# Performance work log

Hardware: AMD Instinct MI355X
Metric: run time of the kernel (lower is better)

The kernel has to match this reference:

```python
import jax, jax.numpy as jnp
import numpy as np

B, C, T, F_, H, HID = 4, 128, 400, 64, 4, 32
CV = C // H  # per-head value channels
EPS = 1e-5


def _head_conv_act_norm(x, W, b, p, g, z):
    # x: [N, C, 2, F]; W: [H, O, C]; b: [H, O]; p: [H] (PReLU); g,z: [H, O, F]
    y = jnp.einsum('hoc,nctf->hnotf', W, x) + b[:, None, :, None, None]
    y = jnp.where(y >= 0, y, p[:, None, None, None, None] * y)  # PReLU (single param per module)
    # LayerNormalization4D over (channel, freq) per (n, t), affine [O, F]
    mu = y.mean(axis=(2, 4), keepdims=True)
    var = y.var(axis=(2, 4), keepdims=True)
    y = (y - mu) / jnp.sqrt(var + EPS)
    return y * g[:, None, :, None, :] + z[:, None, :, None, :]  # [H, N, O, 2, F]


def _conv_act_norm(x, W, b, p, g, z):
    # x: [N, C, 2, F]; W: [O, C]; p: scalar; g,z: [O, F]
    y = jnp.einsum('oc,nctf->notf', W, x) + b[None, :, None, None]
    y = jnp.where(y >= 0, y, p * y)
    mu = y.mean(axis=(1, 3), keepdims=True)
    var = y.var(axis=(1, 3), keepdims=True)
    y = (y - mu) / jnp.sqrt(var + EPS)
    return y * g[None, :, None, :] + z[None, :, None, :]


def setup_inputs() -> dict:
    key = jax.random.key(0)
    ks = jax.random.split(key, 10)
    s = 0.02
    inp = {
        'x1': jax.random.normal(ks[0], (B, C, T, F_), jnp.float32),
        'x2': jax.random.normal(ks[1], (B, C, T, F_), jnp.float32),
        # Query branches (per head)
        'Wq': jax.random.normal(ks[2], (H, HID, C), jnp.float32) * s,
        'bq': jnp.zeros((H, HID), jnp.float32),
        'pq': jnp.full((H,), 0.25, jnp.float32),
        'gq': jnp.ones((H, HID, F_), jnp.float32),
        'zq': jnp.zeros((H, HID, F_), jnp.float32),
        # Key branches
        'Wk': jax.random.normal(ks[3], (H, HID, C), jnp.float32) * s,
        'bk': jnp.zeros((H, HID), jnp.float32),
        'pk': jnp.full((H,), 0.25, jnp.float32),
        'gk': jnp.ones((H, HID, F_), jnp.float32),
        'zk': jnp.zeros((H, HID, F_), jnp.float32),
        # Value branches
        'Wv': jax.random.normal(ks[4], (H, CV, C), jnp.float32) * s,
        'bv': jnp.zeros((H, CV), jnp.float32),
        'pv': jnp.full((H,), 0.25, jnp.float32),
        'gv': jnp.ones((H, CV, F_), jnp.float32),
        'zv': jnp.zeros((H, CV, F_), jnp.float32),
        # Output concat projection
        'Wo': jax.random.normal(ks[5], (C, C), jnp.float32) * s,
        'bo': jnp.zeros((C,), jnp.float32),
        'po': jnp.asarray(0.25, jnp.float32),
        'go': jnp.ones((C, F_), jnp.float32),
        'zo': jnp.zeros((C, F_), jnp.float32),
    }
    return inp


def reference(x1, x2, Wq, bq, pq, gq, zq, Wk, bk, pk, gk, zk, Wv, bv, pv, gv, zv, Wo, bo, po, go, zo):
    N = B * T
    # [B,C,T,F] -> [B*T, C, F]; stack the two streams along a tiny seq axis of 2
    a = x1.transpose(0, 2, 1, 3).reshape(N, C, F_)
    b = x2.transpose(0, 2, 1, 3).reshape(N, C, F_)
    x = jnp.stack([a, b], axis=2)  # [N, C, 2, F]

    Q = _head_conv_act_norm(x, Wq, bq, pq, gq, zq)  # [H, N, HID, 2, F]
    K = _head_conv_act_norm(x, Wk, bk, pk, gk, zk)
    V = _head_conv_act_norm(x, Wv, bv, pv, gv, zv)  # [H, N, CV, 2, F]

    d = HID * F_
    q = Q.transpose(0, 1, 3, 2, 4).reshape(H, N, 2, d)
    k = K.transpose(0, 1, 3, 2, 4).reshape(H, N, 2, d)
    v = V.transpose(0, 1, 3, 2, 4).reshape(H, N, 2, CV * F_)

    attn = jax.nn.softmax(jnp.einsum('hnsd,hntd->hnst', q, k) / (d ** 0.5), axis=-1)  # [H,N,2,2]
    o = jnp.einsum('hnst,hntd->hnsd', attn, v)  # [H, N, 2, CV*F]
    # [H,N,2,CV,F] -> [N, H*CV, 2, F]
    o = o.reshape(H, N, 2, CV, F_).transpose(1, 0, 3, 2, 4).reshape(N, C, 2, F_)

    out = _conv_act_norm(o, Wo, bo, po, go, zo)  # [N, C, 2, F]

    y1 = out[:, :, 0, :].reshape(B, T, C, F_).transpose(0, 2, 1, 3) + x1
    y2 = out[:, :, 1, :].reshape(B, T, C, F_).transpose(0, 2, 1, 3) + x2
    return (y1, y2)
```

## Files before the change

### kernel.cpp

```cpp
#include <hip/hip_runtime.h>


typedef short s8v __attribute__((ext_vector_type(8)));
typedef float f4v __attribute__((ext_vector_type(4)));

__device__ __forceinline__ unsigned short f2bf(float x){
  unsigned u = __float_as_uint(x);
  return (unsigned short)((u + 0x7FFFu + ((u >> 16) & 1u)) >> 16);
}
__device__ __forceinline__ float b2f(unsigned short b){
  return __uint_as_float(((unsigned)b) << 16);
}
__device__ __forceinline__ float wred(float v){
  #pragma unroll
  for (int off = 32; off; off >>= 1) v += __shfl_xor(v, off, 64);
  return v;
}

__global__ __launch_bounds__(256)
void prep_k(const float* __restrict__ Wq, const float* __restrict__ Wk,
            const float* __restrict__ Wv, const float* __restrict__ Wo,
            const float* __restrict__ gq, const float* __restrict__ zq,
            const float* __restrict__ gk, const float* __restrict__ zk,
            const float* __restrict__ gv, const float* __restrict__ zv,
            const float* __restrict__ go, const float* __restrict__ zo,
            unsigned short* __restrict__ Wb, unsigned* __restrict__ GZ)
{
  int t = blockIdx.x * 256 + threadIdx.x;
  if (t < 65536) {
    int sel = t >> 14, i = t & 16383;
    const float* s = sel == 0 ? Wq : sel == 1 ? Wk : sel == 2 ? Wv : Wo;
    Wb[t] = f2bf(s[i]);
  } else {
    int u = t - 65536;
    int sel = u >> 13, i = u & 8191;
    const float* g = sel == 0 ? gq : sel == 1 ? gk : sel == 2 ? gv : go;
    const float* z = sel == 0 ? zq : sel == 1 ? zk : sel == 2 ? zv : zo;
    GZ[u] = (unsigned)f2bf(g[i]) | ((unsigned)f2bf(z[i]) << 16);
  }
}

__device__ __forceinline__ void gemm_tile(const unsigned short* __restrict__ A,
                                          const unsigned short* __restrict__ Bl,
                                          int m0, int n0, int row16, int q4,
                                          f4v acc[2][4])
{
  #pragma unroll
  for (int mi = 0; mi < 2; ++mi)
    #pragma unroll
    for (int ni = 0; ni < 4; ++ni)
      acc[mi][ni] = (f4v){0.f, 0.f, 0.f, 0.f};

  #pragma unroll
  for (int kk = 0; kk < 4; ++kk) {
    s8v a[2];
    #pragma unroll
    for (int mi = 0; mi < 2; ++mi)
      a[mi] = *(const s8v*)(A + (m0 + mi*16 + row16)*128 + kk*32 + q4*8);
    #pragma unroll
    for (int ni = 0; ni < 4; ++ni) {
      int rw = n0 + ni*16 + row16;
      const s8v b = *(const s8v*)(Bl + rw*128 + ((kk*32 + q4*8) ^ ((rw & 7) << 3)));
      #pragma unroll
      for (int mi = 0; mi < 2; ++mi)
        acc[mi][ni] = __builtin_amdgcn_mfma_f32_16x16x32_bf16(a[mi], b, acc[mi][ni], 0, 0, 0);
    }
  }
}

__device__ __forceinline__ void qkv_epi(f4v acc[2][4],
                                        const float* __restrict__ bias,
                                        float p,
                                        const unsigned* __restrict__ GZb,
                                        unsigned short* __restrict__ Lout, bool keep,
                                        int m0, int n0, int row16, int q4)
{
  float sum = 0.f, sq = 0.f;
  #pragma unroll
  for (int mi = 0; mi < 2; ++mi) {
    #pragma unroll
    for (int j = 0; j < 4; ++j) {
      float bb = bias[m0 + mi*16 + q4*4 + j];
      #pragma unroll
      for (int ni = 0; ni < 4; ++ni) {
        float v = acc[mi][ni][j] + bb;
        v = v >= 0.f ? v : p * v;
        acc[mi][ni][j] = v;
        sum += v; sq += v*v;
      }
    }
  }
  sum = wred(sum); sq = wred(sq);
  float mu = sum * (1.f/2048.f);
  float rs = rsqrtf(sq * (1.f/2048.f) - mu*mu + 1e-5f);
  #pragma unroll
  for (int mi = 0; mi < 2; ++mi) {
    #pragma unroll
    for (int ni = 0; ni < 4; ++ni) {
      int f   = ni*16 + row16;
      int col = n0 + f;
      int sw  = (col & 7) << 3;
      #pragma unroll
      for (int j = 0; j < 4; ++j) {
        int r = m0 + mi*16 + q4*4 + j;
        unsigned gz = GZb[r*64 + f];
        float g = b2f((unsigned short)(gz & 0xffffu));
        float z = b2f((unsigned short)(gz >> 16));
        float vn = (acc[mi][ni][j] - mu) * rs * g + z;
        if (keep) acc[mi][ni][j] = vn;
        else      Lout[col*128 + (r ^ sw)] = f2bf(vn);
      }
    }
  }
}

__global__ __launch_bounds__(512, 4)
void fused_k(const float* __restrict__ x1, const float* __restrict__ x2,
             const unsigned short* __restrict__ Wb, const unsigned* __restrict__ GZ,
             const float* __restrict__ bq, const float* __restrict__ bk,
             const float* __restrict__ bv, const float* __restrict__ bo,
             const float* __restrict__ pq, const float* __restrict__ pk,
             const float* __restrict__ pv, const float* __restrict__ po,
             float* __restrict__ out)
{
  __shared__ unsigned short Xl[16384];
  __shared__ unsigned short Kl[16384];
  __shared__ float sc[16];
  __shared__ float lnb[16];

  const int n   = blockIdx.x;
  const int bI  = n / 400, tI = n % 400;
  const int tid = threadIdx.x;
  const int lane = tid & 63, wave = tid >> 6;
  const int wm = wave >> 1, wn = wave & 1;
  const int m0 = wm * 32, n0 = wn * 64;
  const int row16 = lane & 15, q4 = lane >> 4;

  {
    int c = tid & 127, s = (tid >> 7) & 1, half = tid >> 8;
    const float* src = (s ? x2 : x1) + ((size_t)(bI*128 + c)*400 + tI)*64 + half*32;
    #pragma unroll
    for (int j = 0; j < 8; ++j) {
      float4 v = ((const float4*)src)[j];
      int f0 = half*32 + j*4;
      float vv[4] = {v.x, v.y, v.z, v.w};
      #pragma unroll
      for (int e = 0; e < 4; ++e) {
        int rw = s*64 + f0 + e;
        Xl[rw*128 + (c ^ ((rw & 7) << 3))] = f2bf(vv[e]);
      }
    }
  }
  __syncthreads();

  f4v acc[2][4];

  gemm_tile(Wb + 16384*1, Xl, m0, n0, row16, q4, acc);
  qkv_epi(acc, bk, pk[wm], GZ + 8192*1, Kl, false, m0, n0, row16, q4);
  __syncthreads();

  gemm_tile(Wb + 16384*0, Xl, m0, n0, row16, q4, acc);
  qkv_epi(acc, bq, pq[wm], GZ + 8192*0, Kl, true, m0, n0, row16, q4);
  {
    float p0 = 0.f, p1 = 0.f;
    #pragma unroll
    for (int mi = 0; mi < 2; ++mi) {
      #pragma unroll
      for (int ni = 0; ni < 4; ++ni) {
        int f  = ni*16 + row16;
        int sw = (f & 7) << 3;
        #pragma unroll
        for (int j = 0; j < 4; ++j) {
          int r = m0 + mi*16 + q4*4 + j;
          float qv = acc[mi][ni][j];
          float k0 = b2f(Kl[f*128      + (r ^ sw)]);
          float k1 = b2f(Kl[(64+f)*128 + (r ^ sw)]);
          p0 += qv * k0;
          p1 += qv * k1;
        }
      }
    }
    p0 = wred(p0); p1 = wred(p1);
    if (lane == 0) {
      sc[wm*4 + wn*2 + 0] = p0;
      sc[wm*4 + wn*2 + 1] = p1;
    }
  }
  __syncthreads();

  gemm_tile(Wb + 16384*2, Xl, m0, n0, row16, q4, acc);
  qkv_epi(acc, bv, pv[wm], GZ + 8192*2, Kl, false, m0, n0, row16, q4);
  __syncthreads();

  {
    const float is = 0.02209708691f;
    #pragma unroll
    for (int i = 0; i < 2; ++i) {
      int g  = tid + 512*i;
      int f  = g >> 4, cg = g & 15, c0 = cg*8, h = cg >> 2;
      float s00 = sc[h*4+0]*is, s01 = sc[h*4+1]*is;
      float s10 = sc[h*4+2]*is, s11 = sc[h*4+3]*is;
      float mA = fmaxf(s00, s01), e0 = __expf(s00-mA), e1 = __expf(s01-mA);
      float a00 = e0/(e0+e1), a01 = e1/(e0+e1);
      float mB = fmaxf(s10, s11), e2 = __expf(s10-mB), e3 = __expf(s11-mB);
      float a10 = e2/(e2+e3), a11 = e3/(e2+e3);
      int sw = (f & 7) << 3;
      int off0 = f*128      + (c0 ^ sw);
      int off1 = (64+f)*128 + (c0 ^ sw);
      s8v v0 = *(const s8v*)(Kl + off0);
      s8v v1 = *(const s8v*)(Kl + off1);
      s8v o0, o1;
      #pragma unroll
      for (int e = 0; e < 8; ++e) {
        float x0  = b2f((unsigned short)v0[e]);
        float x1v = b2f((unsigned short)v1[e]);
        o0[e] = (short)f2bf(a00*x0 + a01*x1v);
        o1[e] = (short)f2bf(a10*x0 + a11*x1v);
      }
      *(s8v*)(Kl + off0) = o0;
      *(s8v*)(Kl + off1) = o1;
    }
  }
  __syncthreads();

  gemm_tile(Wb + 16384*3, Kl, m0, n0, row16, q4, acc);
  {
    float pov = po[0];
    float sum = 0.f, sq = 0.f;
    #pragma unroll
    for (int mi = 0; mi < 2; ++mi) {
      #pragma unroll
      for (int j = 0; j < 4; ++j) {
        float bb = bo[m0 + mi*16 + q4*4 + j];
        #pragma unroll
        for (int ni = 0; ni < 4; ++ni) {
          float v = acc[mi][ni][j] + bb;
          v = v >= 0.f ? v : pov * v;
          acc[mi][ni][j] = v;
          sum += v; sq += v*v;
        }
      }
    }
    sum = wred(sum); sq = wred(sq);
    if (lane == 0) { lnb[wave] = sum; lnb[8 + wave] = sq; }
    __syncthreads();
    float tot  = lnb[wn]   + lnb[wn+2]   + lnb[wn+4]   + lnb[wn+6];
    float totq = lnb[8+wn] + lnb[8+wn+2] + lnb[8+wn+4] + lnb[8+wn+6];
    float mu = tot * (1.f/8192.f);
    float rs = rsqrtf(totq * (1.f/8192.f) - mu*mu + 1e-5f);
    const unsigned* GZo = GZ + 8192*3;
    float* outs = out + (size_t)wn * 13107200u;
    #pragma unroll
    for (int mi = 0; mi < 2; ++mi) {
      #pragma unroll
      for (int ni = 0; ni < 4; ++ni) {
        int f   = ni*16 + row16;
        int col = n0 + f;
        int sw  = (col & 7) << 3;
        #pragma unroll
        for (int j = 0; j < 4; ++j) {
          int r = m0 + mi*16 + q4*4 + j;
          unsigned gz = GZo[r*64 + f];
          float g = b2f((unsigned short)(gz & 0xffffu));
          float z = b2f((unsigned short)(gz >> 16));
          float y  = (acc[mi][ni][j] - mu) * rs * g + z;
          float xv = b2f(Xl[col*128 + (r ^ sw)]);
          outs[((size_t)(bI*128 + r)*400 + tI)*64 + f] = y + xv;
        }
      }
    }
  }
}

extern "C" void kernel_launch(void* const* d_in, const int* in_sizes, int n_in,
                              void* d_out, int out_size, void* d_ws, size_t ws_size,
                              hipStream_t stream)
{
  (void)in_sizes; (void)n_in; (void)out_size; (void)ws_size;
  const float* x1 = (const float*)d_in[0];
  const float* x2 = (const float*)d_in[1];
  const float* Wq = (const float*)d_in[2];
  const float* bq = (const float*)d_in[3];
  const float* pq = (const float*)d_in[4];
  const float* gq = (const float*)d_in[5];
  const float* zq = (const float*)d_in[6];
  const float* Wk = (const float*)d_in[7];
  const float* bk = (const float*)d_in[8];
  const float* pk = (const float*)d_in[9];
  const float* gk = (const float*)d_in[10];
  const float* zk = (const float*)d_in[11];
  const float* Wv = (const float*)d_in[12];
  const float* bv = (const float*)d_in[13];
  const float* pv = (const float*)d_in[14];
  const float* gv = (const float*)d_in[15];
  const float* zv = (const float*)d_in[16];
  const float* Wo = (const float*)d_in[17];
  const float* bo = (const float*)d_in[18];
  const float* po = (const float*)d_in[19];
  const float* go = (const float*)d_in[20];
  const float* zo = (const float*)d_in[21];

  unsigned short* Wb = (unsigned short*)d_ws;
  unsigned*       GZ = (unsigned*)((char*)d_ws + 131072);

  prep_k<<<384, 256, 0, stream>>>(Wq, Wk, Wv, Wo, gq, zq, gk, zk, gv, zv, go, zo, Wb, GZ);
  fused_k<<<1600, 512, 0, stream>>>(x1, x2, Wb, GZ, bq, bk, bv, bo, pq, pk, pv, po,
                                    (float*)d_out);
}
```

Baseline: 236.3 us.

## Split weights into bf16 hi/lo pairs, keep V in registers, stage output through LDS

Each weight is now stored as a bf16 high part plus a bf16 residual, and every GEMM issues two MFMAs per tile so the weight side is closer to fp32 accuracy. This doubles the MFMA work and the weight loads. The V attention mixing now happens in registers: one wave group hands its values over through fp32 LDS, so the bf16 round-trip through shared memory is gone. The final output is staged through LDS so each stream is written back with coalesced float4 stores instead of scattered scalar stores.

```diff
diff --git a/kernel.cpp b/kernel.cpp
--- a/kernel.cpp
+++ b/kernel.cpp
@@ -30,7 +30,10 @@
   if (t < 65536) {
     int sel = t >> 14, i = t & 16383;
     const float* s = sel == 0 ? Wq : sel == 1 ? Wk : sel == 2 ? Wv : Wo;
-    Wb[t] = f2bf(s[i]);
+    float w = s[i];
+    unsigned short hi = f2bf(w);
+    Wb[t]         = hi;
+    Wb[65536 + t] = f2bf(w - b2f(hi));
   } else {
     int u = t - 65536;
     int sel = u >> 13, i = u & 8191;
@@ -45,6 +48,7 @@
                                           int m0, int n0, int row16, int q4,
                                           f4v acc[2][4])
 {
+  const unsigned short* Al = A + 65536;
   #pragma unroll
   for (int mi = 0; mi < 2; ++mi)
     #pragma unroll
@@ -53,17 +57,22 @@
 
   #pragma unroll
   for (int kk = 0; kk < 4; ++kk) {
-    s8v a[2];
-    #pragma unroll
-    for (int mi = 0; mi < 2; ++mi)
-      a[mi] = *(const s8v*)(A + (m0 + mi*16 + row16)*128 + kk*32 + q4*8);
+    s8v ah[2], al[2];
+    #pragma unroll
+    for (int mi = 0; mi < 2; ++mi) {
+      int off = (m0 + mi*16 + row16)*128 + kk*32 + q4*8;
+      ah[mi] = *(const s8v*)(A  + off);
+      al[mi] = *(const s8v*)(Al + off);
+    }
     #pragma unroll
     for (int ni = 0; ni < 4; ++ni) {
       int rw = n0 + ni*16 + row16;
       const s8v b = *(const s8v*)(Bl + rw*128 + ((kk*32 + q4*8) ^ ((rw & 7) << 3)));
       #pragma unroll
-      for (int mi = 0; mi < 2; ++mi)
-        acc[mi][ni] = __builtin_amdgcn_mfma_f32_16x16x32_bf16(a[mi], b, acc[mi][ni], 0, 0, 0);
+      for (int mi = 0; mi < 2; ++mi) {
+        acc[mi][ni] = __builtin_amdgcn_mfma_f32_16x16x32_bf16(ah[mi], b, acc[mi][ni], 0, 0, 0);
+        acc[mi][ni] = __builtin_amdgcn_mfma_f32_16x16x32_bf16(al[mi], b, acc[mi][ni], 0, 0, 0);
+      }
     }
   }
 }
@@ -123,8 +132,8 @@
              const float* __restrict__ pv, const float* __restrict__ po,
              float* __restrict__ out)
 {
-  __shared__ unsigned short Xl[16384];
-  __shared__ unsigned short Kl[16384];
+  __shared__ __align__(16) unsigned short Xl[16384];
+  __shared__ __align__(16) unsigned short Kl[16384];
   __shared__ float sc[16];
   __shared__ float lnb[16];
 
@@ -189,39 +198,60 @@
   __syncthreads();
 
   gemm_tile(Wb + 16384*2, Xl, m0, n0, row16, q4, acc);
-  qkv_epi(acc, bv, pv[wm], GZ + 8192*2, Kl, false, m0, n0, row16, q4);
-  __syncthreads();
-
-  {
-    const float is = 0.02209708691f;
-    #pragma unroll
-    for (int i = 0; i < 2; ++i) {
-      int g  = tid + 512*i;
-      int f  = g >> 4, cg = g & 15, c0 = cg*8, h = cg >> 2;
-      float s00 = sc[h*4+0]*is, s01 = sc[h*4+1]*is;
-      float s10 = sc[h*4+2]*is, s11 = sc[h*4+3]*is;
+  qkv_epi(acc, bv, pv[wm], GZ + 8192*2, Kl, true, m0, n0, row16, q4);
+
+  {
+    float* KlF = (float*)Kl;
+    if (wn == 0) {
+      #pragma unroll
+      for (int mi = 0; mi < 2; ++mi)
+        #pragma unroll
+        for (int ni = 0; ni < 4; ++ni) {
+          int f = ni*16 + row16;
+          #pragma unroll
+          for (int j = 0; j < 4; ++j)
+            KlF[(m0 + mi*16 + q4*4 + j)*64 + f] = acc[mi][ni][j];
+        }
+    }
+    __syncthreads();
+    float v0r[2][4][4];
+    if (wn == 1) {
+      #pragma unroll
+      for (int mi = 0; mi < 2; ++mi)
+        #pragma unroll
+        for (int ni = 0; ni < 4; ++ni) {
+          int f = ni*16 + row16;
+          #pragma unroll
+          for (int j = 0; j < 4; ++j)
+            v0r[mi][ni][j] = KlF[(m0 + mi*16 + q4*4 + j)*64 + f];
+        }
+    }
+    __syncthreads();
+    if (wn == 1) {
+      const float is = 0.02209708691f;
+      float s00 = sc[wm*4+0]*is, s01 = sc[wm*4+1]*is;
+      float s10 = sc[wm*4+2]*is, s11 = sc[wm*4+3]*is;
       float mA = fmaxf(s00, s01), e0 = __expf(s00-mA), e1 = __expf(s01-mA);
       float a00 = e0/(e0+e1), a01 = e1/(e0+e1);
       float mB = fmaxf(s10, s11), e2 = __expf(s10-mB), e3 = __expf(s11-mB);
       float a10 = e2/(e2+e3), a11 = e3/(e2+e3);
-      int sw = (f & 7) << 3;
-      int off0 = f*128      + (c0 ^ sw);
-      int off1 = (64+f)*128 + (c0 ^ sw);
-      s8v v0 = *(const s8v*)(Kl + off0);
-      s8v v1 = *(const s8v*)(Kl + off1);
-      s8v o0, o1;
-      #pragma unroll
-      for (int e = 0; e < 8; ++e) {
-        float x0  = b2f((unsigned short)v0[e]);
-        float x1v = b2f((unsigned short)v1[e]);
-        o0[e] = (short)f2bf(a00*x0 + a01*x1v);
-        o1[e] = (short)f2bf(a10*x0 + a11*x1v);
-      }
-      *(s8v*)(Kl + off0) = o0;
-      *(s8v*)(Kl + off1) = o1;
-    }
-  }
-  __syncthreads();
+      #pragma unroll
+      for (int mi = 0; mi < 2; ++mi)
+        #pragma unroll
+        for (int ni = 0; ni < 4; ++ni) {
+          int f  = ni*16 + row16;
+          int sw = (f & 7) << 3;
+          #pragma unroll
+          for (int j = 0; j < 4; ++j) {
+            int c = m0 + mi*16 + q4*4 + j;
+            float v0 = v0r[mi][ni][j], v1 = acc[mi][ni][j];
+            Kl[f*128      + (c ^ sw)] = f2bf(a00*v0 + a01*v1);
+            Kl[(64+f)*128 + (c ^ sw)] = f2bf(a10*v0 + a11*v1);
+          }
+        }
+    }
+    __syncthreads();
+  }
 
   gemm_tile(Wb + 16384*3, Kl, m0, n0, row16, q4, acc);
   {
@@ -249,7 +279,6 @@
     float mu = tot * (1.f/8192.f);
     float rs = rsqrtf(totq * (1.f/8192.f) - mu*mu + 1e-5f);
     const unsigned* GZo = GZ + 8192*3;
-    float* outs = out + (size_t)wn * 13107200u;
     #pragma unroll
     for (int mi = 0; mi < 2; ++mi) {
       #pragma unroll
@@ -265,9 +294,40 @@
           float z = b2f((unsigned short)(gz >> 16));
           float y  = (acc[mi][ni][j] - mu) * rs * g + z;
           float xv = b2f(Xl[col*128 + (r ^ sw)]);
-          outs[((size_t)(bI*128 + r)*400 + tI)*64 + f] = y + xv;
-        }
-      }
+          acc[mi][ni][j] = y + xv;
+        }
+      }
+    }
+  }
+
+  {
+    float* KlF = (float*)Kl;
+    const size_t obase = ((size_t)bI * 128 * 400 + (size_t)tI) * 64;
+    #pragma unroll
+    for (int srnd = 0; srnd < 2; ++srnd) {
+      if (wn == srnd) {
+        #pragma unroll
+        for (int mi = 0; mi < 2; ++mi)
+          #pragma unroll
+          for (int ni = 0; ni < 4; ++ni) {
+            int f = ni*16 + row16;
+            #pragma unroll
+            for (int j = 0; j < 4; ++j) {
+              int r = m0 + mi*16 + q4*4 + j;
+              KlF[r*64 + f] = acc[mi][ni][j];
+            }
+          }
+      }
+      __syncthreads();
+      float* outs = out + (size_t)srnd * 13107200u + obase;
+      #pragma unroll
+      for (int k = 0; k < 4; ++k) {
+        int s = k*512 + tid;
+        int r = s >> 4, f4 = (s & 15) * 4;
+        float4 v = *(const float4*)(KlF + r*64 + f4);
+        *(float4*)(outs + (size_t)r * 25600 + f4) = v;
+      }
+      if (srnd == 0) __syncthreads();
     }
   }
 }
@@ -301,7 +361,7 @@
   const float* zo = (const float*)d_in[21];
 
   unsigned short* Wb = (unsigned short*)d_ws;
-  unsigned*       GZ = (unsigned*)((char*)d_ws + 131072);
+  unsigned*       GZ = (unsigned*)((char*)d_ws + 262144);
 
   prep_k<<<384, 256, 0, stream>>>(Wq, Wk, Wv, Wo, gq, zq, gk, zk, gv, zv, go, zo, Wb, GZ);
   fused_k<<<1600, 512, 0, stream>>>(x1, x2, Wb, GZ, bq, bk, bv, bo, pq, pk, pv, po,
```

Result: slower. 323.5 us (+36.9%).

## Split weights into hi/lo bf16 pairs, stage output through LDS for vector stores

Applied to the files above, without the earlier changes.

The weights are now stored as a high bf16 plus a low bf16 residual, and each GEMM issues two MFMAs per tile to recover near-fp32 weight precision. This doubles MFMA work and the A-operand loads. The final output is now written into LDS (reusing Kl as float) one wn-half at a time and then emitted as coalesced float4 nontemporal stores instead of scattered scalar stores. Input loads also switch to nontemporal float4 loads. The extra syncs and the doubled matrix math trade against the better output coalescing.

```diff
diff --git a/kernel.cpp b/kernel.cpp
--- a/kernel.cpp
+++ b/kernel.cpp
@@ -3,6 +3,7 @@
 
 typedef short s8v __attribute__((ext_vector_type(8)));
 typedef float f4v __attribute__((ext_vector_type(4)));
+typedef float fv4 __attribute__((ext_vector_type(4)));
 
 __device__ __forceinline__ unsigned short f2bf(float x){
   unsigned u = __float_as_uint(x);
@@ -30,7 +31,10 @@
   if (t < 65536) {
     int sel = t >> 14, i = t & 16383;
     const float* s = sel == 0 ? Wq : sel == 1 ? Wk : sel == 2 ? Wv : Wo;
-    Wb[t] = f2bf(s[i]);
+    float w = s[i];
+    unsigned short hi = f2bf(w);
+    Wb[t]         = hi;
+    Wb[65536 + t] = f2bf(w - b2f(hi));
   } else {
     int u = t - 65536;
     int sel = u >> 13, i = u & 8191;
@@ -45,6 +49,7 @@
                                           int m0, int n0, int row16, int q4,
                                           f4v acc[2][4])
 {
+  const unsigned short* Al = A + 65536;
   #pragma unroll
   for (int mi = 0; mi < 2; ++mi)
     #pragma unroll
@@ -53,17 +58,22 @@
 
   #pragma unroll
   for (int kk = 0; kk < 4; ++kk) {
-    s8v a[2];
-    #pragma unroll
-    for (int mi = 0; mi < 2; ++mi)
-      a[mi] = *(const s8v*)(A + (m0 + mi*16 + row16)*128 + kk*32 + q4*8);
+    s8v ah[2], al[2];
+    #pragma unroll
+    for (int mi = 0; mi < 2; ++mi) {
+      int off = (m0 + mi*16 + row16)*128 + kk*32 + q4*8;
+      ah[mi] = *(const s8v*)(A  + off);
+      al[mi] = *(const s8v*)(Al + off);
+    }
     #pragma unroll
     for (int ni = 0; ni < 4; ++ni) {
       int rw = n0 + ni*16 + row16;
       const s8v b = *(const s8v*)(Bl + rw*128 + ((kk*32 + q4*8) ^ ((rw & 7) << 3)));
       #pragma unroll
-      for (int mi = 0; mi < 2; ++mi)
-        acc[mi][ni] = __builtin_amdgcn_mfma_f32_16x16x32_bf16(a[mi], b, acc[mi][ni], 0, 0, 0);
+      for (int mi = 0; mi < 2; ++mi) {
+        acc[mi][ni] = __builtin_amdgcn_mfma_f32_16x16x32_bf16(ah[mi], b, acc[mi][ni], 0, 0, 0);
+        acc[mi][ni] = __builtin_amdgcn_mfma_f32_16x16x32_bf16(al[mi], b, acc[mi][ni], 0, 0, 0);
+      }
     }
   }
 }
@@ -123,8 +133,8 @@
              const float* __restrict__ pv, const float* __restrict__ po,
              float* __restrict__ out)
 {
-  __shared__ unsigned short Xl[16384];
-  __shared__ unsigned short Kl[16384];
+  __shared__ __align__(16) unsigned short Xl[16384];
+  __shared__ __align__(16) unsigned short Kl[16384];
   __shared__ float sc[16];
   __shared__ float lnb[16];
 
@@ -141,13 +151,12 @@
     const float* src = (s ? x2 : x1) + ((size_t)(bI*128 + c)*400 + tI)*64 + half*32;
     #pragma unroll
     for (int j = 0; j < 8; ++j) {
-      float4 v = ((const float4*)src)[j];
+      fv4 v = __builtin_nontemporal_load(((const fv4*)src) + j);
       int f0 = half*32 + j*4;
-      float vv[4] = {v.x, v.y, v.z, v.w};
       #pragma unroll
       for (int e = 0; e < 4; ++e) {
         int rw = s*64 + f0 + e;
-        Xl[rw*128 + (c ^ ((rw & 7) << 3))] = f2bf(vv[e]);
+        Xl[rw*128 + (c ^ ((rw & 7) << 3))] = f2bf(v[e]);
       }
     }
   }
@@ -249,7 +258,6 @@
     float mu = tot * (1.f/8192.f);
     float rs = rsqrtf(totq * (1.f/8192.f) - mu*mu + 1e-5f);
     const unsigned* GZo = GZ + 8192*3;
-    float* outs = out + (size_t)wn * 13107200u;
     #pragma unroll
     for (int mi = 0; mi < 2; ++mi) {
       #pragma unroll
@@ -265,9 +273,40 @@
           float z = b2f((unsigned short)(gz >> 16));
           float y  = (acc[mi][ni][j] - mu) * rs * g + z;
           float xv = b2f(Xl[col*128 + (r ^ sw)]);
-          outs[((size_t)(bI*128 + r)*400 + tI)*64 + f] = y + xv;
+          acc[mi][ni][j] = y + xv;
         }
       }
+    }
+  }
+
+  {
+    float* KlF = (float*)Kl;
+    const size_t obase = ((size_t)bI * 128 * 400 + (size_t)tI) * 64;
+    #pragma unroll
+    for (int srnd = 0; srnd < 2; ++srnd) {
+      if (wn == srnd) {
+        #pragma unroll
+        for (int mi = 0; mi < 2; ++mi)
+          #pragma unroll
+          for (int ni = 0; ni < 4; ++ni) {
+            int f = ni*16 + row16;
+            #pragma unroll
+            for (int j = 0; j < 4; ++j) {
+              int r = m0 + mi*16 + q4*4 + j;
+              KlF[r*64 + f] = acc[mi][ni][j];
+            }
+          }
+      }
+      __syncthreads();
+      float* outs = out + (size_t)srnd * 13107200u + obase;
+      #pragma unroll
+      for (int k = 0; k < 4; ++k) {
+        int s = k*512 + tid;
+        int r = s >> 4, f4 = (s & 15) * 4;
+        fv4 v = *(const fv4*)(KlF + r*64 + f4);
+        __builtin_nontemporal_store(v, (fv4*)(outs + (size_t)r * 25600 + f4));
+      }
+      if (srnd == 0) __syncthreads();
     }
   }
 }
@@ -301,7 +340,7 @@
   const float* zo = (const float*)d_in[21];
 
   unsigned short* Wb = (unsigned short*)d_ws;
-  unsigned*       GZ = (unsigned*)((char*)d_ws + 131072);
+  unsigned*       GZ = (unsigned*)((char*)d_ws + 262144);
 
   prep_k<<<384, 256, 0, stream>>>(Wq, Wk, Wv, Wo, gq, zq, gk, zk, gv, zv, go, zo, Wb, GZ);
   fused_k<<<1600, 512, 0, stream>>>(x1, x2, Wb, GZ, bq, bk, bv, bo, pq, pk, pv, po,
```

Measured after the change: 349.3 us. +47.9%, slower.
